# Optimization experiments

Measured on AMD Instinct MI355X. Metric: run time of the kernel, lower is better.

## Reference

```python
import jax, jax.numpy as jnp
import numpy as np

N = 50000          # nodes
E = 800000         # edges (avg in-degree 16)
IN_FEATS = 256
H = 4              # num_heads
D = 32             # out_feats per head
NEG_SLOPE = 0.2


def setup_inputs() -> dict:
    key = jax.random.key(0)
    k1, k2, k3, k4, k5, k6 = jax.random.split(key, 6)
    feat = jax.random.normal(k1, (N, IN_FEATS), dtype=jnp.float32)
    src = jax.random.randint(k2, (E,), 0, N, dtype=jnp.int32)
    dst = jax.random.randint(k3, (E,), 0, N, dtype=jnp.int32)
    # parameters (xavier-ish scale)
    W = jax.random.normal(k4, (IN_FEATS, H * D), dtype=jnp.float32) * (2.0 / (IN_FEATS + H * D)) ** 0.5
    attn_l = jax.random.normal(k5, (H, D), dtype=jnp.float32) * 0.1
    attn_r = jax.random.normal(k6, (H, D), dtype=jnp.float32) * 0.1
    bias = jnp.zeros((H * D,), dtype=jnp.float32)
    return {"feat": feat, "src": src, "dst": dst, "W": W,
            "attn_l": attn_l, "attn_r": attn_r, "bias": bias}


def reference(feat, src, dst, W, attn_l, attn_r, bias):
    # dense projection: [N, H, D]
    ft = (feat @ W).reshape(N, H, D)
    # per-node attention logits: [N, H]
    el = jnp.einsum('nhd,hd->nh', ft, attn_l)
    er = jnp.einsum('nhd,hd->nh', ft, attn_r)
    # SDDMM u_add_v + leaky relu: per-edge scores [E, H]
    e = jax.nn.leaky_relu(el[src] + er[dst], negative_slope=NEG_SLOPE)
    # edge softmax over incoming edges of each dst node (segment softmax)
    m = jax.ops.segment_max(e, dst, num_segments=N)          # [N, H], -inf for empty
    e_exp = jnp.exp(e - m[dst])                               # [E, H]
    s = jax.ops.segment_sum(e_exp, dst, num_segments=N)       # [N, H]
    a = e_exp / s[dst]                                        # [E, H]
    # SpMM u_mul_e: weighted aggregation to dst nodes
    rst = jax.ops.segment_sum(ft[src] * a[:, :, None], dst, num_segments=N)  # [N, H, D]
    rst = rst + bias.reshape(1, H, D)
    return rst
```

## Files before the change

### kernel.cpp

```cpp
#include <hip/hip_runtime.h>
#include <hip/hip_bf16.h>
#include <math.h>

#define N_NODES 50000
#define N_EDGES 800000
#define IN_F 256
#define HD 128
#define NHEAD 4
#define NB_SCAN 196
#define GBM 64

typedef __attribute__((ext_vector_type(8))) short bf16x8;
typedef __attribute__((ext_vector_type(4))) float f32x4;

__device__ __forceinline__ float lrelu(float x){ return x > 0.f ? x : 0.2f * x; }

__device__ __forceinline__ unsigned short f32_to_bf16_rn(float x){
    union { float f; unsigned int u; } v; v.f = x;
    unsigned int r = v.u + 0x7FFFu + ((v.u >> 16) & 1u);
    return (unsigned short)(r >> 16);
}
__device__ __forceinline__ float bf16_to_f32(unsigned short h){
    union { unsigned int u; float f; } v; v.u = ((unsigned int)h) << 16;
    return v.f;
}
__device__ __forceinline__ float bflo(unsigned int u){
    union { unsigned int x; float f; } v; v.x = u << 16; return v.f;
}
__device__ __forceinline__ float bfhi(unsigned int u){
    union { unsigned int x; float f; } v; v.x = u & 0xFFFF0000u; return v.f;
}

__global__ __launch_bounds__(256) void prep_kernel(const float* __restrict__ W,
                                                   unsigned short* __restrict__ Wt_hi,
                                                   unsigned short* __restrict__ Wt_lo,
                                                   int* __restrict__ deg){
    int b = blockIdx.x;
    if (b < NB_SCAN){
        int i = b * 256 + threadIdx.x;
        if (i < N_NODES) deg[i] = 0;
    } else {
        int gid = (b - NB_SCAN) * 256 + threadIdx.x;
        int n = gid >> 8;
        int k = gid & 255;
        float x = W[(size_t)k * HD + n];
        unsigned short h = f32_to_bf16_rn(x);
        float r = x - bf16_to_f32(h);
        Wt_hi[gid] = h;
        Wt_lo[gid] = f32_to_bf16_rn(r);
    }
}

__global__ __launch_bounds__(256, 4) void gemm_kernel(const float* __restrict__ feat,
                                                      const unsigned short* __restrict__ Wt_hi,
                                                      const unsigned short* __restrict__ Wt_lo,
                                                      const float* __restrict__ attn_l,
                                                      const float* __restrict__ attn_r,
                                                      unsigned short* __restrict__ ftb,
                                                      float* __restrict__ el,
                                                      float* __restrict__ er){
    const int tid  = threadIdx.x;
    const int lane = tid & 63;
    const int wv   = tid >> 6;
    const int r    = lane & 15;
    const int g    = lane >> 4;
    const int arow = blockIdx.x * GBM + wv * 16 + r;
    const bool rowok = (arow < N_NODES);
    const float* arp = feat + (size_t)arow * IN_F + g * 8;
    const unsigned short* bhp = Wt_hi + r * 256 + g * 8;
    const unsigned short* blp = Wt_lo + r * 256 + g * 8;

    f32x4 acc[8];
#pragma unroll
    for (int j = 0; j < 8; ++j) acc[j] = (f32x4){0.f, 0.f, 0.f, 0.f};

    float4 a0 = make_float4(0.f,0.f,0.f,0.f), a1 = a0;
    if (rowok){ a0 = *(const float4*)(arp); a1 = *(const float4*)(arp + 4); }

#pragma unroll
    for (int t = 0; t < 8; ++t){
        float4 n0 = make_float4(0.f,0.f,0.f,0.f), n1 = n0;
        if (t < 7 && rowok){
            n0 = *(const float4*)(arp + (t + 1) * 32);
            n1 = *(const float4*)(arp + (t + 1) * 32 + 4);
        }
        float av[8] = {a0.x, a0.y, a0.z, a0.w, a1.x, a1.y, a1.z, a1.w};
        bf16x8 ah, al;
#pragma unroll
        for (int j = 0; j < 8; ++j){
            unsigned short h = f32_to_bf16_rn(av[j]);
            ah[j] = (short)h;
            al[j] = (short)f32_to_bf16_rn(av[j] - bf16_to_f32(h));
        }
        const unsigned short* bh_t = bhp + t * 32;
        const unsigned short* bl_t = blp + t * 32;
#pragma unroll
        for (int nf = 0; nf < 8; ++nf){
            bf16x8 bh = *(const bf16x8*)(bh_t + nf * 4096);
            bf16x8 bl = *(const bf16x8*)(bl_t + nf * 4096);
            acc[nf] = __builtin_amdgcn_mfma_f32_16x16x32_bf16(ah, bh, acc[nf], 0, 0, 0);
            acc[nf] = __builtin_amdgcn_mfma_f32_16x16x32_bf16(ah, bl, acc[nf], 0, 0, 0);
            acc[nf] = __builtin_amdgcn_mfma_f32_16x16x32_bf16(al, bh, acc[nf], 0, 0, 0);
        }
        a0 = n0; a1 = n1;
    }
    float alv[8], arv[8];
#pragma unroll
    for (int nf = 0; nf < 8; ++nf){
        alv[nf] = attn_l[r + nf * 16];
        arv[nf] = attn_r[r + nf * 16];
    }
    const int g4 = g * 4;
#pragma unroll
    for (int rg = 0; rg < 4; ++rg){
        int gr = blockIdx.x * GBM + wv * 16 + g4 + rg;
        if (gr < N_NODES){
            unsigned short* op = ftb + (size_t)gr * HD + r;
#pragma unroll
            for (int nf = 0; nf < 8; ++nf) op[nf * 16] = f32_to_bf16_rn(acc[nf][rg]);
        }
        float pl0 = acc[0][rg] * alv[0] + acc[1][rg] * alv[1];
        float pl1 = acc[2][rg] * alv[2] + acc[3][rg] * alv[3];
        float pl2 = acc[4][rg] * alv[4] + acc[5][rg] * alv[5];
        float pl3 = acc[6][rg] * alv[6] + acc[7][rg] * alv[7];
        float pr0 = acc[0][rg] * arv[0] + acc[1][rg] * arv[1];
        float pr1 = acc[2][rg] * arv[2] + acc[3][rg] * arv[3];
        float pr2 = acc[4][rg] * arv[4] + acc[5][rg] * arv[5];
        float pr3 = acc[6][rg] * arv[6] + acc[7][rg] * arv[7];
#pragma unroll
        for (int m = 1; m <= 8; m <<= 1){
            pl0 += __shfl_xor(pl0, m, 64); pl1 += __shfl_xor(pl1, m, 64);
            pl2 += __shfl_xor(pl2, m, 64); pl3 += __shfl_xor(pl3, m, 64);
            pr0 += __shfl_xor(pr0, m, 64); pr1 += __shfl_xor(pr1, m, 64);
            pr2 += __shfl_xor(pr2, m, 64); pr3 += __shfl_xor(pr3, m, 64);
        }
        if (r == 0 && gr < N_NODES){
            *(float4*)(el + (size_t)gr * NHEAD) = make_float4(pl0, pl1, pl2, pl3);
            *(float4*)(er + (size_t)gr * NHEAD) = make_float4(pr0, pr1, pr2, pr3);
        }
    }
}

__global__ void degree_kernel(const int* __restrict__ dst, int* __restrict__ deg,
                              int* __restrict__ rank){
    int e = blockIdx.x * blockDim.x + threadIdx.x;
    if (e < N_EDGES) rank[e] = atomicAdd(&deg[dst[e]], 1);
}

__global__ __launch_bounds__(256) void scan_part(const int* __restrict__ deg,
                                                 int* __restrict__ row_off,
                                                 int* __restrict__ blk_sums){
    __shared__ int lds[256];
    int tid = threadIdx.x;
    int i = blockIdx.x * 256 + tid;
    int v = (i < N_NODES) ? deg[i] : 0;
    int x = v;
    lds[tid] = x;
    __syncthreads();
    for (int off = 1; off < 256; off <<= 1){
        int t = (tid >= off) ? lds[tid - off] : 0;
        __syncthreads();
        x += t;
        lds[tid] = x;
        __syncthreads();
    }
    if (i < N_NODES) row_off[i] = x - v;
    if (tid == 255) blk_sums[blockIdx.x] = x;
}

__global__ __launch_bounds__(256) void scan_mid(int* __restrict__ blk_sums,
                                                int* __restrict__ blk_off){
    __shared__ int lds[256];
    int tid = threadIdx.x;
    int v = (tid < NB_SCAN) ? blk_sums[tid] : 0;
    int x = v;
    lds[tid] = x;
    __syncthreads();
    for (int off = 1; off < 256; off <<= 1){
        int t = (tid >= off) ? lds[tid - off] : 0;
        __syncthreads();
        x += t;
        lds[tid] = x;
        __syncthreads();
    }
    blk_off[tid] = x - v;
}

__global__ __launch_bounds__(256) void scan_add(int* __restrict__ row_off,
                                                const int* __restrict__ blk_off){
    int i = blockIdx.x * 256 + threadIdx.x;
    if (i < N_NODES) row_off[i] += blk_off[blockIdx.x];
    if (blockIdx.x == 0 && threadIdx.x == 0) row_off[N_NODES] = N_EDGES;
}

__global__ void scatter_kernel(const int* __restrict__ src, const int* __restrict__ dst,
                               const int* __restrict__ rank, const int* __restrict__ row_off,
                               int* __restrict__ csr_src){
    int e = blockIdx.x * blockDim.x + threadIdx.x;
    if (e >= N_EDGES) return;
    csr_src[row_off[dst[e]] + rank[e]] = src[e];
}

__global__ __launch_bounds__(256) void aggregate_kernel(const unsigned short* __restrict__ ftb,
                                                        const int* __restrict__ csr_src,
                                                        const float* __restrict__ el,
                                                        const float* __restrict__ er,
                                                        const int* __restrict__ row_off,
                                                        const float* __restrict__ bias,
                                                        float* __restrict__ out){
    __shared__ float lw[4][4][16][4];
    __shared__ int   ls[4][4][16];

    const int wv   = threadIdx.x >> 6;
    const int lane = threadIdx.x & 63;
    const int grp  = lane >> 4;
    const int l    = lane & 15;
    const int h    = l >> 2;
    const int n    = blockIdx.x * 16 + wv * 4 + grp;
    const int beg  = row_off[n], end = row_off[n + 1];
    const float4 ern = *(const float4*)(er + (size_t)n * NHEAD);

    float a[8];
#pragma unroll
    for (int k = 0; k < 8; ++k) a[k] = 0.f;
    float wsum = 0.f;

    for (int base = beg; base < end; base += 16){
        int cnt = end - base; if (cnt > 16) cnt = 16;
        if (l < cnt){
            int s_l = csr_src[base + l];
            float4 elv = *(const float4*)(el + (size_t)s_l * NHEAD);
            float4 w4;
            w4.x = __expf(lrelu(elv.x + ern.x));
            w4.y = __expf(lrelu(elv.y + ern.y));
            w4.z = __expf(lrelu(elv.z + ern.z));
            w4.w = __expf(lrelu(elv.w + ern.w));
            ls[wv][grp][l] = s_l;
            *(float4*)(&lw[wv][grp][l][0]) = w4;
        }
        asm volatile("s_waitcnt lgkmcnt(0)" ::: "memory");
        __builtin_amdgcn_sched_barrier(0);
        for (int j = 0; j < cnt; ++j){
            float w = lw[wv][grp][j][h];
            int   s = ls[wv][grp][j];
            uint4 f = *(const uint4*)(ftb + (size_t)s * HD + 8 * l);
            a[0] += w * bflo(f.x); a[1] += w * bfhi(f.x);
            a[2] += w * bflo(f.y); a[3] += w * bfhi(f.y);
            a[4] += w * bflo(f.z); a[5] += w * bfhi(f.z);
            a[6] += w * bflo(f.w); a[7] += w * bfhi(f.w);
            wsum += w;
        }
        __builtin_amdgcn_sched_barrier(0);
    }
    float inv = (end > beg) ? 1.f / wsum : 0.f;
    float4 b0 = *(const float4*)(bias + 8 * l);
    float4 b1 = *(const float4*)(bias + 8 * l + 4);
    float4 o0, o1;
    o0.x = a[0] * inv + b0.x; o0.y = a[1] * inv + b0.y;
    o0.z = a[2] * inv + b0.z; o0.w = a[3] * inv + b0.w;
    o1.x = a[4] * inv + b1.x; o1.y = a[5] * inv + b1.y;
    o1.z = a[6] * inv + b1.z; o1.w = a[7] * inv + b1.w;
    *(float4*)(out + (size_t)n * HD + 8 * l)     = o0;
    *(float4*)(out + (size_t)n * HD + 8 * l + 4) = o1;
}

extern "C" void kernel_launch(void* const* d_in, const int* in_sizes, int n_in,
                              void* d_out, int out_size, void* d_ws, size_t ws_size,
                              hipStream_t stream){
    const float* feat   = (const float*)d_in[0];
    const int*   src    = (const int*)  d_in[1];
    const int*   dst    = (const int*)  d_in[2];
    const float* W      = (const float*)d_in[3];
    const float* attn_l = (const float*)d_in[4];
    const float* attn_r = (const float*)d_in[5];
    const float* bias   = (const float*)d_in[6];
    float* out = (float*)d_out;
    char*  ws  = (char*)d_ws;

    unsigned short* ftb = (unsigned short*)(ws + 0);
    float* el      = (float*)(ws + 12800000);
    float* er      = (float*)(ws + 13600000);
    int*   deg     = (int*)  (ws + 14400000);
    int*   rank    = (int*)  (ws + 14600000);
    int*   row_off = (int*)  (ws + 17800000);
    int*   csr_src = (int*)  (ws + 18000064);
    unsigned short* Wt_hi = (unsigned short*)(ws + 21200064);
    unsigned short* Wt_lo = (unsigned short*)(ws + 21265600);

    int* blk_sums = (int*)csr_src;
    int* blk_off  = blk_sums + 256;

    prep_kernel<<<NB_SCAN + 128, 256, 0, stream>>>(W, Wt_hi, Wt_lo, deg);
    gemm_kernel<<<(N_NODES + GBM - 1) / GBM, 256, 0, stream>>>(feat, Wt_hi, Wt_lo,
                                                               attn_l, attn_r, ftb, el, er);
    degree_kernel<<<(N_EDGES + 255) / 256, 256, 0, stream>>>(dst, deg, rank);
    scan_part<<<NB_SCAN, 256, 0, stream>>>(deg, row_off, blk_sums);
    scan_mid<<<1, 256, 0, stream>>>(blk_sums, blk_off);
    scan_add<<<NB_SCAN, 256, 0, stream>>>(row_off, blk_off);
    scatter_kernel<<<(N_EDGES + 255) / 256, 256, 0, stream>>>(src, dst, rank, row_off, csr_src);
    aggregate_kernel<<<N_NODES / 16, 256, 0, stream>>>(ftb, csr_src, el, er,
                                                       row_off, bias, out);
}
```

Baseline: 253.3 us.

## Drop W low-part split and stage bf16 weights in LDS for GEMM

The projection GEMM no longer splits W into hi/lo bf16 parts; it uses only the bf16-rounded W and keeps the hi/lo split on the activations, cutting the MFMAs per tile from three to two. The weight tile is now staged cooperatively into shared memory in 64-wide K chunks, with barriers, instead of each wave reading it from global memory. This lowers MFMA count and global/L2 traffic for W, but the bf16 truncation of W reduces projection accuracy and the added syncs may limit overlap.

```diff
diff --git a/kernel.cpp b/kernel.cpp
--- a/kernel.cpp
+++ b/kernel.cpp
@@ -33,7 +33,6 @@
 
 __global__ __launch_bounds__(256) void prep_kernel(const float* __restrict__ W,
                                                    unsigned short* __restrict__ Wt_hi,
-                                                   unsigned short* __restrict__ Wt_lo,
                                                    int* __restrict__ deg){
     int b = blockIdx.x;
     if (b < NB_SCAN){
@@ -43,22 +42,19 @@
         int gid = (b - NB_SCAN) * 256 + threadIdx.x;
         int n = gid >> 8;
         int k = gid & 255;
-        float x = W[(size_t)k * HD + n];
-        unsigned short h = f32_to_bf16_rn(x);
-        float r = x - bf16_to_f32(h);
-        Wt_hi[gid] = h;
-        Wt_lo[gid] = f32_to_bf16_rn(r);
+        Wt_hi[gid] = f32_to_bf16_rn(W[(size_t)k * HD + n]);
     }
 }
 
 __global__ __launch_bounds__(256, 4) void gemm_kernel(const float* __restrict__ feat,
                                                       const unsigned short* __restrict__ Wt_hi,
-                                                      const unsigned short* __restrict__ Wt_lo,
                                                       const float* __restrict__ attn_l,
                                                       const float* __restrict__ attn_r,
                                                       unsigned short* __restrict__ ftb,
                                                       float* __restrict__ el,
                                                       float* __restrict__ er){
+    __shared__ unsigned short Bh[2][8][64][8];
+
     const int tid  = threadIdx.x;
     const int lane = tid & 63;
     const int wv   = tid >> 6;
@@ -67,42 +63,61 @@
     const int arow = blockIdx.x * GBM + wv * 16 + r;
     const bool rowok = (arow < N_NODES);
     const float* arp = feat + (size_t)arow * IN_F + g * 8;
-    const unsigned short* bhp = Wt_hi + r * 256 + g * 8;
-    const unsigned short* blp = Wt_lo + r * 256 + g * 8;
 
     f32x4 acc[8];
 #pragma unroll
     for (int j = 0; j < 8; ++j) acc[j] = (f32x4){0.f, 0.f, 0.f, 0.f};
 
-    float4 a0 = make_float4(0.f,0.f,0.f,0.f), a1 = a0;
-    if (rowok){ a0 = *(const float4*)(arp); a1 = *(const float4*)(arp + 4); }
-
-#pragma unroll
-    for (int t = 0; t < 8; ++t){
-        float4 n0 = make_float4(0.f,0.f,0.f,0.f), n1 = n0;
-        if (t < 7 && rowok){
-            n0 = *(const float4*)(arp + (t + 1) * 32);
-            n1 = *(const float4*)(arp + (t + 1) * 32 + 4);
-        }
-        float av[8] = {a0.x, a0.y, a0.z, a0.w, a1.x, a1.y, a1.z, a1.w};
-        bf16x8 ah, al;
-#pragma unroll
-        for (int j = 0; j < 8; ++j){
-            unsigned short h = f32_to_bf16_rn(av[j]);
-            ah[j] = (short)h;
-            al[j] = (short)f32_to_bf16_rn(av[j] - bf16_to_f32(h));
-        }
-        const unsigned short* bh_t = bhp + t * 32;
-        const unsigned short* bl_t = blp + t * 32;
-#pragma unroll
-        for (int nf = 0; nf < 8; ++nf){
-            bf16x8 bh = *(const bf16x8*)(bh_t + nf * 4096);
-            bf16x8 bl = *(const bf16x8*)(bl_t + nf * 4096);
-            acc[nf] = __builtin_amdgcn_mfma_f32_16x16x32_bf16(ah, bh, acc[nf], 0, 0, 0);
-            acc[nf] = __builtin_amdgcn_mfma_f32_16x16x32_bf16(ah, bl, acc[nf], 0, 0, 0);
-            acc[nf] = __builtin_amdgcn_mfma_f32_16x16x32_bf16(al, bh, acc[nf], 0, 0, 0);
-        }
-        a0 = n0; a1 = n1;
+    float4 a[4];
+#pragma unroll
+    for (int j = 0; j < 4; ++j) a[j] = make_float4(0.f, 0.f, 0.f, 0.f);
+    if (rowok){
+        a[0] = *(const float4*)(arp);      a[1] = *(const float4*)(arp + 4);
+        a[2] = *(const float4*)(arp + 32); a[3] = *(const float4*)(arp + 36);
+    }
+
+    for (int kc = 0; kc < 4; ++kc){
+        const int k0 = kc * 64;
+#pragma unroll
+        for (int i = 0; i < 4; ++i){
+            int u  = i * 256 + tid;
+            int l2 = u & 63;
+            int fn = (u >> 6) & 7;
+            int kb = u >> 9;
+            int nn = fn * 16 + (l2 & 15);
+            int kk = k0 + kb * 32 + (l2 >> 4) * 8;
+            *(uint4*)(&Bh[kb][fn][l2][0]) = *(const uint4*)(Wt_hi + nn * 256 + kk);
+        }
+        __syncthreads();
+        float4 n[4];
+#pragma unroll
+        for (int j = 0; j < 4; ++j) n[j] = make_float4(0.f, 0.f, 0.f, 0.f);
+        if (kc < 3 && rowok){
+            const float* np = arp + (kc + 1) * 64;
+            n[0] = *(const float4*)(np);      n[1] = *(const float4*)(np + 4);
+            n[2] = *(const float4*)(np + 32); n[3] = *(const float4*)(np + 36);
+        }
+#pragma unroll
+        for (int kb = 0; kb < 2; ++kb){
+            float av[8] = {a[2*kb].x, a[2*kb].y, a[2*kb].z, a[2*kb].w,
+                           a[2*kb+1].x, a[2*kb+1].y, a[2*kb+1].z, a[2*kb+1].w};
+            bf16x8 ah, al;
+#pragma unroll
+            for (int j = 0; j < 8; ++j){
+                unsigned short h = f32_to_bf16_rn(av[j]);
+                ah[j] = (short)h;
+                al[j] = (short)f32_to_bf16_rn(av[j] - bf16_to_f32(h));
+            }
+#pragma unroll
+            for (int nf = 0; nf < 8; ++nf){
+                bf16x8 bh = *(const bf16x8*)(&Bh[kb][nf][lane][0]);
+                acc[nf] = __builtin_amdgcn_mfma_f32_16x16x32_bf16(ah, bh, acc[nf], 0, 0, 0);
+                acc[nf] = __builtin_amdgcn_mfma_f32_16x16x32_bf16(al, bh, acc[nf], 0, 0, 0);
+            }
+        }
+        __syncthreads();
+#pragma unroll
+        for (int j = 0; j < 4; ++j) a[j] = n[j];
     }
     float alv[8], arv[8];
 #pragma unroll
@@ -285,13 +300,12 @@
     int*   row_off = (int*)  (ws + 17800000);
     int*   csr_src = (int*)  (ws + 18000064);
     unsigned short* Wt_hi = (unsigned short*)(ws + 21200064);
-    unsigned short* Wt_lo = (unsigned short*)(ws + 21265600);
 
     int* blk_sums = (int*)csr_src;
     int* blk_off  = blk_sums + 256;
 
-    prep_kernel<<<NB_SCAN + 128, 256, 0, stream>>>(W, Wt_hi, Wt_lo, deg);
-    gemm_kernel<<<(N_NODES + GBM - 1) / GBM, 256, 0, stream>>>(feat, Wt_hi, Wt_lo,
+    prep_kernel<<<NB_SCAN + 128, 256, 0, stream>>>(W, Wt_hi, deg);
+    gemm_kernel<<<(N_NODES + GBM - 1) / GBM, 256, 0, stream>>>(feat, Wt_hi,
                                                                attn_l, attn_r, ftb, el, er);
     degree_kernel<<<(N_EDGES + 255) / 256, 256, 0, stream>>>(dst, deg, rank);
     scan_part<<<NB_SCAN, 256, 0, stream>>>(deg, row_off, blk_sums);
```

Result: faster. 207.7 us (-18.0%).
